# Performance work log

Measured on AMD Instinct MI355X. Metric: run time of the kernel, lower is better.

Reference implementation:

```python
import jax, jax.numpy as jnp
import numpy as np

N, E = 4096, 65536
H = 200
KS = (3072, 1536, 768)  # ceil(0.75*4096), ceil(0.5*3072), ceil(0.5*1536)


def _gcn(A, x, W, b):
    # GCNConv with improved=True: A_hat = A + 2I, sym-normalized
    n = A.shape[0]
    Ah = A + 2.0 * jnp.eye(n, dtype=A.dtype)
    dinv = jax.lax.rsqrt(Ah.sum(axis=1))
    An = dinv[:, None] * Ah * dinv[None, :]
    return An @ (x @ W) + b


def _augment(A):
    # GraphUNet.augment_adj: remove self loops, add self loops (w=1), spspmm(A,A), remove self loops
    n = A.shape[0]
    eye = jnp.eye(n, dtype=A.dtype)
    Ap = A * (1.0 - eye) + eye
    A2 = Ap @ Ap  # dense form of spspmm (two-hop adjacency with weights)
    return A2 * (1.0 - eye)


def _pool(A, x, pw, k):
    # TopKPooling: score = tanh(x.w/||w||), keep top-k, scale kept x by score
    score = jnp.tanh((x @ pw) / jnp.linalg.norm(pw))
    val, perm = jax.lax.top_k(score, k)
    return x[perm] * val[:, None], A[perm][:, perm], perm


def _unet(x, adj, w0, b0, w1, b1, w2, b2, w3, b3, p1, p2, p3,
          u0w, u0b, u1w, u1b, u2w, u2b):
    down = [(w1, b1), (w2, b2), (w3, b3)]
    pws = [p1, p2, p3]
    up = [(u0w, u0b), (u1w, u1b), (u2w, u2b)]
    x = jax.nn.relu(_gcn(adj, x, w0, b0))
    xs, As, perms = [x], [adj], []
    A = adj
    for i in range(3):
        A = _augment(A)
        x, A, perm = _pool(A, x, pws[i], KS[i])
        x = jax.nn.relu(_gcn(A, x, *down[i]))
        if i < 2:
            xs.append(x)
            As.append(A)
        perms.append(perm)
    for i in range(3):
        j = 2 - i
        upf = jnp.zeros_like(xs[j]).at[perms[j]].set(x)
        x = xs[j] + upf  # sum_res=True
        x = _gcn(As[j], x, *up[i])
        if i < 2:
            x = jax.nn.relu(x)
    return jax.nn.log_softmax(x, axis=1)


def setup_inputs() -> dict:
    key = jax.random.key(0)
    ks = jax.random.split(key, 16)
    x = jax.random.normal(ks[0], (N, 3), dtype=jnp.float32)
    src = jax.random.randint(ks[1], (E,), 0, N)
    dst = jax.random.randint(ks[2], (E,), 0, N)
    A = jnp.zeros((N, N), jnp.float32).at[src, dst].set(1.0)
    A = jnp.maximum(A, A.T) * (1.0 - jnp.eye(N, dtype=jnp.float32))
    g = lambda k, s: jax.random.normal(k, s, jnp.float32) * 0.1
    z = lambda n: jnp.zeros((n,), jnp.float32)
    return dict(
        x=x, adj=A,
        w0=g(ks[3], (3, H)), b0=z(H),
        w1=g(ks[4], (H, H)), b1=z(H),
        w2=g(ks[5], (H, H)), b2=z(H),
        w3=g(ks[6], (H, H)), b3=z(H),
        p1=g(ks[7], (H,)), p2=g(ks[8], (H,)), p3=g(ks[9], (H,)),
        u0w=g(ks[10], (H, H)), u0b=z(H),
        u1w=g(ks[11], (H, H)), u1b=z(H),
        u2w=g(ks[12], (H, 2)), u2b=z(2),
    )


def reference(x, adj, w0, b0, w1, b1, w2, b2, w3, b3, p1, p2, p3,
              u0w, u0b, u1w, u1b, u2w, u2b):
    return _unet(x, adj, w0, b0, w1, b1, w2, b2, w3, b3, p1, p2, p3,
                 u0w, u0b, u1w, u1b, u2w, u2b)
```

## Files before the change

### kernel.cpp

```cpp
#include <hip/hip_runtime.h>

typedef unsigned short u16;
typedef unsigned int u32;
typedef unsigned long long u64;
typedef signed char s8;
typedef __attribute__((ext_vector_type(8))) short bfrag8;
typedef __attribute__((ext_vector_type(4))) float f32x4;
typedef __attribute__((ext_vector_type(4))) int i32x4;
typedef __attribute__((address_space(1))) const void gconst_void;
typedef __attribute__((address_space(3))) void lds_void_t;

__device__ __forceinline__ float bf2f(u16 u) {
  return __uint_as_float(((u32)u) << 16);
}
__device__ __forceinline__ u16 f2bf(float f) {
  u32 u = __float_as_uint(f);
  u32 r = (u + 0x7FFFu + ((u >> 16) & 1u)) >> 16;
  return (u16)r;
}
__device__ __forceinline__ void split3(float v, u16& hi, u16& mi, u16& lo) {
  hi = f2bf(v); float r1 = v - bf2f(hi);
  mi = f2bf(r1); float r2 = r1 - bf2f(mi);
  lo = f2bf(r2);
}
__device__ __forceinline__ float ld1(const void* p, int isbf, long idx) {
  return isbf ? bf2f(((const u16*)p)[idx]) : ((const float*)p)[idx];
}
__device__ __forceinline__ void ld4(const void* p, int isbf, long base, long gc, long bound, float v[4]) {
  if (gc + 3 < bound && ((base & 3) == 0)) {
    if (isbf) {
      const ushort4 u = *(const ushort4*)((const u16*)p + base);
      v[0] = bf2f(u.x); v[1] = bf2f(u.y); v[2] = bf2f(u.z); v[3] = bf2f(u.w);
    } else {
      const float4 f = *(const float4*)((const float*)p + base);
      v[0] = f.x; v[1] = f.y; v[2] = f.z; v[3] = f.w;
    }
  } else {
    #pragma unroll
    for (int d = 0; d < 4; ++d) v[d] = (gc + d < bound) ? ld1(p, isbf, base + d) : 0.f;
  }
}

__global__ void detect_k(const u32* __restrict__ a, long nw, int* __restrict__ flag) {
  long stride = (long)gridDim.x * 256;
  int f = 0;
  for (long j = (long)blockIdx.x * 256 + threadIdx.x; j < nw; j += stride) {
    u32 w = a[j];
    if (w == 0x00003F80u || w == 0x3F803F80u) f = 1;
  }
  if (__any(f)) {
    if ((threadIdx.x & 63) == 0) atomicOr(flag, 1);
  }
}

__device__ __forceinline__ int get_bf(int abf, const int* dtf) {
  return (abf >= 0) ? abf : *dtf;
}

__device__ __forceinline__ void stageB16(const void* g, void* lds) {
#if __has_builtin(__builtin_amdgcn_global_load_lds)
  __builtin_amdgcn_global_load_lds((gconst_void*)g, (lds_void_t*)lds, 16, 0, 0);
#else
  int lane = threadIdx.x & 63;
  *(int4*)((char*)lds + lane * 16) = *(const int4*)g;
#endif
}

__global__ __launch_bounds__(256) void syrk_tri_i8_parts(
    const s8* __restrict__ Ag, int ldk, int Ksplit, int ntri,
    int* __restrict__ parts)
{
  __shared__ s8 At[128 * 64];
  __shared__ s8 Bt[128 * 64];
  const int t = blockIdx.x;
  int ti = (int)((sqrtf((float)(8 * t + 1)) - 1.0f) * 0.5f);
  while ((ti + 1) * (ti + 2) / 2 <= t) ++ti;
  while (ti * (ti + 1) / 2 > t) --ti;
  const int tj = t - ti * (ti + 1) / 2;

  const int tid = threadIdx.x;
  const int wave = tid >> 6, lane = tid & 63;
  const int wr = wave >> 1, wc = wave & 1;
  const long rowA0 = (long)ti * 128;
  const long rowB0 = (long)tj * 128;
  const int kbeg = blockIdx.y * Ksplit;
  const int kend = kbeg + Ksplit;

  i32x4 acc[4][4];
  #pragma unroll
  for (int i = 0; i < 4; ++i)
    #pragma unroll
    for (int j = 0; j < 4; ++j) acc[i][j] = (i32x4)0;

  const int srow = lane >> 2;
  const int scol = (lane & 3) * 16;
  const int m = lane & 15, q = lane >> 4;

  for (int k0 = kbeg; k0 < kend; k0 += 64) {
    #pragma unroll
    for (int tt = 0; tt < 2; ++tt) {
      const int r = wave * 32 + tt * 16;
      stageB16(Ag + (rowA0 + r + srow) * (long)ldk + k0 + scol, At + r * 64);
      stageB16(Ag + (rowB0 + r + srow) * (long)ldk + k0 + scol, Bt + r * 64);
    }
    __syncthreads();

    i32x4 af[4], bf[4];
    #pragma unroll
    for (int mt = 0; mt < 4; ++mt)
      af[mt] = *(const i32x4*)(At + (wr * 64 + mt * 16 + m) * 64 + q * 16);
    #pragma unroll
    for (int nt = 0; nt < 4; ++nt)
      bf[nt] = *(const i32x4*)(Bt + (wc * 64 + nt * 16 + m) * 64 + q * 16);
    #pragma unroll
    for (int mt = 0; mt < 4; ++mt)
      #pragma unroll
      for (int nt = 0; nt < 4; ++nt)
        acc[mt][nt] = __builtin_amdgcn_mfma_i32_16x16x64_i8(af[mt], bf[nt], acc[mt][nt], 0, 0, 0);
    __syncthreads();
  }

  int* P = parts + ((long)blockIdx.y * ntri + t) * 16384;
  #pragma unroll
  for (int mt = 0; mt < 4; ++mt) {
    #pragma unroll
    for (int nt = 0; nt < 4; ++nt) {
      const int r0 = wr * 64 + mt * 16 + q * 4;
      const int c = wc * 64 + nt * 16 + m;
      #pragma unroll
      for (int r = 0; r < 4; ++r)
        P[(r0 + r) * 128 + c] = acc[mt][nt][r];
    }
  }
}

__global__ __launch_bounds__(256) void reduce_tri_i8_k(
    const int* __restrict__ parts, int ntri, int n, int nz,
    u16* __restrict__ Ah, u16* __restrict__ Al)
{
  __shared__ float T[128 * 33];
  const int t = blockIdx.x >> 2;
  const int slab = blockIdx.x & 3;
  int ti = (int)((sqrtf((float)(8 * t + 1)) - 1.0f) * 0.5f);
  while ((ti + 1) * (ti + 2) / 2 <= t) ++ti;
  while (ti * (ti + 1) / 2 > t) --ti;
  const int tj = t - ti * (ti + 1) / 2;
  const long rowA0 = (long)ti * 128;
  const long rowB0 = (long)tj * 128;
  const int r0 = slab * 32;
  const int tid = threadIdx.x;
  const long tstride = (long)ntri * 16384;

  #pragma unroll
  for (int it = 0; it < 16; ++it) {
    const int idx = it * 256 + tid;
    const int lr = idx >> 7;
    const int lc = idx & 127;
    long base = (long)t * 16384 + (r0 + lr) * 128 + lc;
    int v = 0;
    for (int z = 0; z < nz; ++z) v += parts[(long)z * tstride + base];
    const long gr = rowA0 + r0 + lr;
    const long gc = rowB0 + lc;
    if (gr == gc) v = 0;
    const float fv = (float)v;
    const u16 h = f2bf(fv);
    const long o = gr * n + gc;
    Ah[o] = h;
    if (Al) Al[o] = f2bf(fv - bf2f(h));
    T[lc * 33 + lr] = fv;
  }
  if (ti == tj) return;
  __syncthreads();
  #pragma unroll
  for (int it = 0; it < 16; ++it) {
    const int idx = it * 256 + tid;
    const int mr = idx >> 5;
    const int mc = idx & 31;
    const float fv = T[mr * 33 + mc];
    const u16 h = f2bf(fv);
    const long o = (rowB0 + mr) * n + rowA0 + r0 + mc;
    Ah[o] = h;
    if (Al) Al[o] = f2bf(fv - bf2f(h));
  }
}

__global__ void rowsum_planes_k(const u16* __restrict__ Ah, const u16* __restrict__ Al,
                                int n, double* __restrict__ rs) {
  __shared__ double red[256];
  const int row = blockIdx.x, tid = threadIdx.x;
  const uint4* A4 = (const uint4*)(Ah + (long)row * n);
  const uint4* L4 = Al ? (const uint4*)(Al + (long)row * n) : nullptr;
  const int n8 = n >> 3;
  double s = 0.0;
  for (int j = tid; j < n8; j += 256) {
    uint4 u = A4[j];
    float v = bf2f((u16)(u.x & 0xFFFFu)) + bf2f((u16)(u.x >> 16))
            + bf2f((u16)(u.y & 0xFFFFu)) + bf2f((u16)(u.y >> 16))
            + bf2f((u16)(u.z & 0xFFFFu)) + bf2f((u16)(u.z >> 16))
            + bf2f((u16)(u.w & 0xFFFFu)) + bf2f((u16)(u.w >> 16));
    if (L4) {
      uint4 l = L4[j];
      v += bf2f((u16)(l.x & 0xFFFFu)) + bf2f((u16)(l.x >> 16))
         + bf2f((u16)(l.y & 0xFFFFu)) + bf2f((u16)(l.y >> 16))
         + bf2f((u16)(l.z & 0xFFFFu)) + bf2f((u16)(l.z >> 16))
         + bf2f((u16)(l.w & 0xFFFFu)) + bf2f((u16)(l.w >> 16));
    }
    s += (double)v;
  }
  red[tid] = s; __syncthreads();
  for (int st = 128; st > 0; st >>= 1) {
    if (tid < st) red[tid] += red[tid + st];
    __syncthreads();
  }
  if (tid == 0) rs[row] = red[0];
}

__global__ __launch_bounds__(256) void syrk_tri2_parts(
    const u16* __restrict__ Ah, const u16* __restrict__ Al, int ldk,
    float* __restrict__ parts, int n, int per)
{
  __shared__ u16 Ath[128 * 32];
  __shared__ u16 Bth[128 * 32];
  __shared__ u16 Atl[128 * 32];
  __shared__ u16 Btl[128 * 32];
  const int t = blockIdx.x;
  int ti = (int)((sqrtf((float)(8 * t + 1)) - 1.0f) * 0.5f);
  while ((ti + 1) * (ti + 2) / 2 <= t) ++ti;
  while (ti * (ti + 1) / 2 > t) --ti;
  const int tj = t - ti * (ti + 1) / 2;

  const int tid = threadIdx.x;
  const int wave = tid >> 6, lane = tid & 63;
  const int wr = wave >> 1, wc = wave & 1;
  const long rowA0 = (long)ti * 128;
  const long rowB0 = (long)tj * 128;
  const int kbeg = blockIdx.y * per;
  const int kend = kbeg + per;

  f32x4 acc[4][4];
  #pragma unroll
  for (int i = 0; i < 4; ++i)
    #pragma unroll
    for (int j = 0; j < 4; ++j) acc[i][j] = (f32x4)0.f;

  const int srow = lane >> 2;
  const int scol = (lane & 3) * 8;
  const int m = lane & 15, q = lane >> 4;

  for (int k0 = kbeg; k0 < kend; k0 += 32) {
    #pragma unroll
    for (int tt = 0; tt < 2; ++tt) {
      const int r = wave * 32 + tt * 16;
      stageB16(Ah + (rowA0 + r + srow) * (long)ldk + k0 + scol, Ath + r * 32);
      stageB16(Ah + (rowB0 + r + srow) * (long)ldk + k0 + scol, Bth + r * 32);
      stageB16(Al + (rowA0 + r + srow) * (long)ldk + k0 + scol, Atl + r * 32);
      stageB16(Al + (rowB0 + r + srow) * (long)ldk + k0 + scol, Btl + r * 32);
    }
    __syncthreads();

    bfrag8 afh[4], afl[4], bfh[4], bfl[4];
    #pragma unroll
    for (int mt = 0; mt < 4; ++mt) {
      afh[mt] = *(const bfrag8*)(Ath + (wr * 64 + mt * 16 + m) * 32 + q * 8);
      afl[mt] = *(const bfrag8*)(Atl + (wr * 64 + mt * 16 + m) * 32 + q * 8);
    }
    #pragma unroll
    for (int nt = 0; nt < 4; ++nt) {
      bfh[nt] = *(const bfrag8*)(Bth + (wc * 64 + nt * 16 + m) * 32 + q * 8);
      bfl[nt] = *(const bfrag8*)(Btl + (wc * 64 + nt * 16 + m) * 32 + q * 8);
    }
    #pragma unroll
    for (int mt = 0; mt < 4; ++mt)
      #pragma unroll
      for (int nt = 0; nt < 4; ++nt) {
        acc[mt][nt] = __builtin_amdgcn_mfma_f32_16x16x32_bf16(afh[mt], bfh[nt], acc[mt][nt], 0, 0, 0);
        acc[mt][nt] = __builtin_amdgcn_mfma_f32_16x16x32_bf16(afh[mt], bfl[nt], acc[mt][nt], 0, 0, 0);
        acc[mt][nt] = __builtin_amdgcn_mfma_f32_16x16x32_bf16(afl[mt], bfh[nt], acc[mt][nt], 0, 0, 0);
        acc[mt][nt] = __builtin_amdgcn_mfma_f32_16x16x32_bf16(afl[mt], bfl[nt], acc[mt][nt], 0, 0, 0);
      }
    __syncthreads();
  }

  float* P = parts + (long)blockIdx.y * n * n;
  #pragma unroll
  for (int mt = 0; mt < 4; ++mt) {
    #pragma unroll
    for (int nt = 0; nt < 4; ++nt) {
      const long gr0 = rowA0 + wr * 64 + mt * 16 + q * 4;
      const long gc = rowB0 + wc * 64 + nt * 16 + m;
      #pragma unroll
      for (int r = 0; r < 4; ++r)
        P[(gr0 + r) * n + gc] = acc[mt][nt][r];
    }
  }
}

__global__ void reduce_tri_mirror_k(const float* __restrict__ parts,
                                    u16* __restrict__ Ah, u16* __restrict__ Al,
                                    double* __restrict__ rsum, int n, int nz) {
  __shared__ double red[256];
  const int tid = threadIdx.x;
  long idx = (long)blockIdx.x * 256 + tid;
  long nn = (long)n * n;
  long r = idx / n, c = idx - r * n;
  double myv = 0.0;
  if (idx < nn) {
    if (r == c) {
      Ah[idx] = 0; Al[idx] = 0;
    } else if (r > c) {
      float s = 0.f;
      for (int z = 0; z < nz; ++z) s += parts[(long)z * nn + r * n + c];
      long mi = c * n + r;
      u16 h = f2bf(s);
      u16 l = f2bf(s - bf2f(h));
      Ah[idx] = h; Al[idx] = l;
      Ah[mi] = h;  Al[mi] = l;
      myv = (double)s;
      atomicAdd(&rsum[c], (double)s);
    }
  }
  red[tid] = myv;
  __syncthreads();
  for (int st = 128; st > 0; st >>= 1) {
    if (tid < st) red[tid] += red[tid + st];
    __syncthreads();
  }
  if (tid == 0 && idx < nn) atomicAdd(&rsum[r], red[0]);
}

__global__ void bg_i8_k(const void* __restrict__ src, int srcbf, int nsrc,
                        const int* __restrict__ perm, int kRows,
                        s8* __restrict__ Ag, const int* __restrict__ dtf,
                        const float* __restrict__ xsrc, const float* __restrict__ score,
                        float* __restrict__ xdst, unsigned nbB) {
  if (blockIdx.x < nbB) {
    long tot = (long)kRows * nsrc;
    long idx = (long)blockIdx.x * 256 + threadIdx.x;
    if (idx >= tot) return;
    int r = (int)(idx / nsrc);
    int c = (int)(idx - (long)r * nsrc);
    int p = perm[r];
    float v = ld1(src, get_bf(srcbf, dtf), (long)p * nsrc + c);
    if (c == p) v += 1.f;
    Ag[idx] = (s8)(int)v;
  } else {
    long tot = (long)kRows * 200;
    long idx = (long)(blockIdx.x - nbB) * 256 + threadIdx.x;
    if (idx >= tot) return;
    int r = (int)(idx / 200);
    int c = (int)(idx - (long)r * 200);
    int p = perm[r];
    xdst[idx] = xsrc[(long)p * 200 + c] * score[p];
  }
}

__global__ void bg_sp_k(const u16* __restrict__ srcH, const u16* __restrict__ srcL,
                        int nsrc, const int* __restrict__ perm, int kRows,
                        u16* __restrict__ Agh, u16* __restrict__ Agl,
                        const float* __restrict__ xsrc, const float* __restrict__ score,
                        float* __restrict__ xdst, unsigned nbB) {
  if (blockIdx.x < nbB) {
    long tot = (long)kRows * nsrc;
    long idx = (long)blockIdx.x * 256 + threadIdx.x;
    if (idx >= tot) return;
    int r = (int)(idx / nsrc);
    int c = (int)(idx - (long)r * nsrc);
    int p = perm[r];
    long si = (long)p * nsrc + c;
    float v = bf2f(srcH[si]) + bf2f(srcL[si]);
    if (c == p) v += 1.f;
    u16 h = f2bf(v);
    Agh[idx] = h;
    Agl[idx] = f2bf(v - bf2f(h));
  } else {
    long tot = (long)kRows * 200;
    long idx = (long)(blockIdx.x - nbB) * 256 + threadIdx.x;
    if (idx >= tot) return;
    int r = (int)(idx / 200);
    int c = (int)(idx - (long)r * 200);
    int p = perm[r];
    xdst[idx] = xsrc[(long)p * 200 + c] * score[p];
  }
}

template<int NT>
__global__ __launch_bounds__(256) void agg_mfma(
    const u16* __restrict__ Ah, const u16* __restrict__ Al,
    const u16* __restrict__ ZT, float* __restrict__ parts,
    int K, int per_steps)
{
  __shared__ u16 At[128 * 32];
  __shared__ u16 Alt[128 * 32];
  __shared__ u16 Zt[3 * NT * 512];
  const int tid = threadIdx.x;
  const int wave = tid >> 6, lane = tid & 63;
  const long row0 = (long)blockIdx.x * 128;
  const int chunk = blockIdx.y;
  const int kbeg = chunk * per_steps * 32;
  const int kend = min(K, kbeg + per_steps * 32);
  const int m = lane & 15, q = lane >> 4;
  const int srow = lane >> 2, scol = (lane & 3) * 8;
  const bool hasAl = (Al != nullptr);

  f32x4 acc[2][NT];
  #pragma unroll
  for (int rt = 0; rt < 2; ++rt)
    #pragma unroll
    for (int ct = 0; ct < NT; ++ct) acc[rt][ct] = (f32x4)0.f;

  for (int k0 = kbeg; k0 < kend; k0 += 32) {
    #pragma unroll
    for (int t = 0; t < 2; ++t) {
      const int r = wave * 32 + t * 16;
      stageB16(Ah + (row0 + r + srow) * (long)K + k0 + scol, At + r * 32);
      if (hasAl)
        stageB16(Al + (row0 + r + srow) * (long)K + k0 + scol, Alt + r * 32);
    }
    for (int s = wave; s < 3 * NT; s += 4) {
      const u16* g = ZT + ((long)(s * 16 + srow)) * K + k0 + scol;
      stageB16(g, Zt + s * 512);
    }
    __syncthreads();

    bfrag8 af0 = *(const bfrag8*)(At + (wave * 32 + m) * 32 + q * 8);
    bfrag8 af1 = *(const bfrag8*)(At + (wave * 32 + 16 + m) * 32 + q * 8);
    bfrag8 al0, al1;
    if (hasAl) {
      al0 = *(const bfrag8*)(Alt + (wave * 32 + m) * 32 + q * 8);
      al1 = *(const bfrag8*)(Alt + (wave * 32 + 16 + m) * 32 + q * 8);
    }
    #pragma unroll
    for (int ct = 0; ct < NT; ++ct) {
      bfrag8 b0 = *(const bfrag8*)(Zt + (0 * NT + ct) * 512 + m * 32 + q * 8);
      bfrag8 b1 = *(const bfrag8*)(Zt + (1 * NT + ct) * 512 + m * 32 + q * 8);
      bfrag8 b2 = *(const bfrag8*)(Zt + (2 * NT + ct) * 512 + m * 32 + q * 8);
      acc[0][ct] = __builtin_amdgcn_mfma_f32_16x16x32_bf16(af0, b0, acc[0][ct], 0, 0, 0);
      acc[0][ct] = __builtin_amdgcn_mfma_f32_16x16x32_bf16(af0, b1, acc[0][ct], 0, 0, 0);
      acc[0][ct] = __builtin_amdgcn_mfma_f32_16x16x32_bf16(af0, b2, acc[0][ct], 0, 0, 0);
      acc[1][ct] = __builtin_amdgcn_mfma_f32_16x16x32_bf16(af1, b0, acc[1][ct], 0, 0, 0);
      acc[1][ct] = __builtin_amdgcn_mfma_f32_16x16x32_bf16(af1, b1, acc[1][ct], 0, 0, 0);
      acc[1][ct] = __builtin_amdgcn_mfma_f32_16x16x32_bf16(af1, b2, acc[1][ct], 0, 0, 0);
      if (hasAl) {
        acc[0][ct] = __builtin_amdgcn_mfma_f32_16x16x32_bf16(al0, b0, acc[0][ct], 0, 0, 0);
        acc[0][ct] = __builtin_amdgcn_mfma_f32_16x16x32_bf16(al0, b1, acc[0][ct], 0, 0, 0);
        acc[1][ct] = __builtin_amdgcn_mfma_f32_16x16x32_bf16(al1, b0, acc[1][ct], 0, 0, 0);
        acc[1][ct] = __builtin_amdgcn_mfma_f32_16x16x32_bf16(al1, b1, acc[1][ct], 0, 0, 0);
      }
    }
    __syncthreads();
  }

  float* P = parts + (long)chunk * gridDim.x * 128 * (NT * 16);
  #pragma unroll
  for (int rt = 0; rt < 2; ++rt) {
    #pragma unroll
    for (int ct = 0; ct < NT; ++ct) {
      const long grow0 = row0 + wave * 32 + rt * 16 + q * 4;
      const long gcol = ct * 16 + m;
      #pragma unroll
      for (int r = 0; r < 4; ++r)
        P[(grow0 + r) * (NT * 16) + gcol] = acc[rt][ct][r];
    }
  }
}

__global__ __launch_bounds__(256) void reduce_epi_k(
    const float* __restrict__ parts, const float* __restrict__ Zs,
    const double* __restrict__ rs, const float* __restrict__ b,
    float* __restrict__ out, int n, int nz, int relu,
    const float* __restrict__ pw, float* __restrict__ score)
{
  __shared__ float vrow[200];
  const int i = blockIdx.x, tid = threadIdx.x;
  float dv = (float)(1.0 / sqrt(rs[i] + 2.0));
  if (tid < 200) {
    long base = (long)i * 208 + tid;
    float s = 0.f;
    for (int c = 0; c < nz; ++c) s += parts[(long)c * n * 208 + base];
    float v = dv * (s + 2.f * Zs[(long)i * 200 + tid]) + b[tid];
    if (relu) v = fmaxf(v, 0.f);
    out[(long)i * 200 + tid] = v;
    if (score) vrow[tid] = v;
  }
  if (!score) return;
  __syncthreads();
  if (tid < 64) {
    double ps = 0.0;
    for (int j = tid; j < 200; j += 64) { double w = pw[j]; ps += w * w; }
    for (int off = 32; off > 0; off >>= 1) ps += __shfl_down(ps, off);
    double nrm = sqrt(__shfl(ps, 0));
    double s = 0.0;
    for (int j = tid; j < 200; j += 64) s += (double)vrow[j] * (double)pw[j];
    for (int off = 32; off > 0; off >>= 1) s += __shfl_down(s, off);
    if (tid == 0) score[i] = (float)tanh(s / nrm);
  }
}

__global__ void a_from_adj_rs_k(const void* __restrict__ adj, const int* __restrict__ dtf,
                                int n, u16* __restrict__ Ah, double* __restrict__ rs) {
  __shared__ double red[256];
  int bf = *dtf;
  const int row = blockIdx.x, tid = threadIdx.x;
  const long base = (long)row * n;
  double s = 0.0;
  for (int j = tid; j < n; j += 256) {
    float v = ld1(adj, bf, base + j);
    Ah[base + j] = bf ? ((const u16*)adj)[base + j] : f2bf(v);
    s += (double)v;
  }
  red[tid] = s; __syncthreads();
  for (int st = 128; st > 0; st >>= 1) {
    if (tid < st) red[tid] += red[tid + st];
    __syncthreads();
  }
  if (tid == 0) rs[row] = red[0];
}

__global__ __launch_bounds__(256) void gemm64_f64(
    const void* __restrict__ Ap, long lda, int abf,
    const void* __restrict__ Bp, long ldb, int bbf,
    float* __restrict__ C, long ldc, int M, int N, int K,
    const double* __restrict__ rsum, u16* __restrict__ ZT, const int* __restrict__ dtf)
{
  const int abf_ = get_bf(abf, dtf);
  const int bbf_ = get_bf(bbf, dtf);
  __shared__ float As[16][64];
  __shared__ float Bs[16][64];
  const int tid = threadIdx.x;
  const int tr = tid >> 4, tc = tid & 15;
  const long row0 = (long)blockIdx.y * 64;
  const long col0 = (long)blockIdx.x * 64;
  double acc[4][4];
  #pragma unroll
  for (int i = 0; i < 4; ++i)
    #pragma unroll
    for (int j = 0; j < 4; ++j) acc[i][j] = 0.0;

  const int am = tid >> 2;
  const int ak = (tid & 3) * 4;
  const int bk = tid >> 4;
  const int bn = (tid & 15) * 4;

  for (int k0 = 0; k0 < K; k0 += 16) {
    float va[4] = {0.f, 0.f, 0.f, 0.f};
    {
      long gm = row0 + am; long gk = k0 + ak;
      if (gm < M && gk < K) ld4(Ap, abf_, gm * lda + gk, gk, K, va);
    }
    As[ak + 0][am] = va[0]; As[ak + 1][am] = va[1];
    As[ak + 2][am] = va[2]; As[ak + 3][am] = va[3];

    float vb[4] = {0.f, 0.f, 0.f, 0.f};
    {
      long gk = k0 + bk; long gn = col0 + bn;
      if (gk < K && gn < N) ld4(Bp, bbf_, gk * ldb + gn, gn, N, vb);
    }
    Bs[bk][bn + 0] = vb[0]; Bs[bk][bn + 1] = vb[1];
    Bs[bk][bn + 2] = vb[2]; Bs[bk][bn + 3] = vb[3];

    __syncthreads();
    #pragma unroll
    for (int kk = 0; kk < 16; ++kk) {
      float a[4], b[4];
      #pragma unroll
      for (int i = 0; i < 4; ++i) a[i] = As[kk][tr * 4 + i];
      #pragma unroll
      for (int j = 0; j < 4; ++j) b[j] = Bs[kk][tc * 4 + j];
      #pragma unroll
      for (int i = 0; i < 4; ++i)
        #pragma unroll
        for (int j = 0; j < 4; ++j)
          acc[i][j] += (double)a[i] * (double)b[j];
    }
    __syncthreads();
  }
  #pragma unroll
  for (int i = 0; i < 4; ++i) {
    long gm = row0 + tr * 4 + i;
    if (gm >= M) continue;
    float sc = rsum ? (float)(1.0 / sqrt(rsum[gm] + 2.0)) : 1.f;
    #pragma unroll
    for (int j = 0; j < 4; ++j) {
      long gn = col0 + tc * 4 + j;
      if (gn < N) {
        float v0 = (float)acc[i][j];
        float v = v0 * sc;
        C[gm * ldc + gn] = v;
        if (ZT) {
          u16 hi, mi, lo; split3(v, hi, mi, lo);
          ZT[((long)0 * 208 + gn) * M + gm] = hi;
          ZT[((long)1 * 208 + gn) * M + gm] = mi;
          ZT[((long)2 * 208 + gn) * M + gm] = lo;
        }
      }
    }
  }
}

struct UpBatch {
  const void* src[19];
  float* dst[19];
  int n[19];
};

__global__ void upcast_batch_k(UpBatch ub, const int* __restrict__ dtf) {
  int bf = *dtf;
  int a = blockIdx.y;
  int i = blockIdx.x * 256 + threadIdx.x;
  if (i < ub.n[a]) ub.dst[a][i] = ld1(ub.src[a], bf, i);
}

template<int V>
__global__ __launch_bounds__(1024) void topk_fast(const float* __restrict__ score,
                                                  int n, int np2, int k,
                                                  int* __restrict__ perm,
                                                  int* __restrict__ inv) {
  __shared__ u64 keys[4096];
  const int tid = threadIdx.x;
  const int REGMAX = 32 * V;
  for (int i = tid; i < n; i += 1024) inv[i] = -1;
  u64 kreg[V];
  #pragma unroll
  for (int r = 0; r < V; ++r) {
    int i = tid * V + r;
    u64 key = 0ULL;
    if (i < n) {
      u32 b = __float_as_uint(score[i]);
      u32 u = (b & 0x80000000u) ? ~b : (b | 0x80000000u);
      key = ((u64)u << 32) | (u32)(~(u32)i);
    }
    kreg[r] = key;
  }

  for (int size = 2; size <= np2; size <<= 1) {
    int stride = size >> 1;
    if (stride > REGMAX) {
      #pragma unroll
      for (int r = 0; r < V; ++r) keys[tid * V + r] = kreg[r];
      __syncthreads();
      for (; stride > REGMAX; stride >>= 1) {
        for (int i = tid; i < np2; i += 1024) {
          int j = i ^ stride;
          if (j > i) {
            u64 a = keys[i], b = keys[j];
            bool up = ((i & size) == 0);
            if (up ? (a > b) : (a < b)) { keys[i] = b; keys[j] = a; }
          }
        }
        __syncthreads();
      }
      #pragma unroll
      for (int r = 0; r < V; ++r) kreg[r] = keys[tid * V + r];
    }
    for (; stride >= 1; stride >>= 1) {
      if (stride >= V) {
        int lm = stride / V;
        #pragma unroll
        for (int r = 0; r < V; ++r) {
          u64 mine = kreg[r];
          u64 other = (u64)__shfl_xor((long long)mine, lm);
          int i = tid * V + r;
          bool up = ((i & size) == 0);
          bool lower = ((i & stride) == 0);
          u64 mn = mine < other ? mine : other;
          u64 mx = mine < other ? other : mine;
          kreg[r] = (lower == up) ? mn : mx;
        }
      } else {
        #pragma unroll
        for (int r = 0; r < V; ++r) {
          int pr = r ^ stride;
          if (pr > r) {
            int i = tid * V + r;
            bool up = ((i & size) == 0);
            u64 a = kreg[r], b = kreg[pr];
            if (up ? (a > b) : (a < b)) { kreg[r] = b; kreg[pr] = a; }
          }
        }
      }
    }
  }
  #pragma unroll
  for (int r = 0; r < V; ++r) {
    int i = tid * V + r;
    int rank = np2 - 1 - i;
    if (rank < k) {
      int idx = (int)(~(u32)(kreg[r] & 0xFFFFFFFFull));
      perm[rank] = idx;
      inv[idx] = rank;
    }
  }
}

__global__ void upadd_k(const float* __restrict__ xs, const float* __restrict__ xpool,
                        const int* __restrict__ inv, float* __restrict__ dst, long nh, int h) {
  long idx = (long)blockIdx.x * 256 + threadIdx.x;
  if (idx >= nh) return;
  int i = (int)(idx / h);
  int c = (int)(idx - (long)i * h);
  float v = xs[idx];
  int r = inv[i];
  if (r >= 0) v += xpool[(long)r * h + c];
  dst[idx] = v;
}

__global__ void matvec2_final_k(const void* __restrict__ A, int abf, int n,
                                const float* __restrict__ Zs, const double* __restrict__ rs0,
                                const float* __restrict__ b2, float* __restrict__ out,
                                const int* __restrict__ dtf) {
  const int bf = get_bf(abf, dtf);
  int row = blockIdx.x, tid = threadIdx.x;
  const long base = (long)row * n;
  double s0 = 0.0, s1 = 0.0;
  for (int j = tid; j < n; j += 256) {
    double a = (double)ld1(A, bf, base + j);
    s0 += a * (double)Zs[2 * j];
    s1 += a * (double)Zs[2 * j + 1];
  }
  __shared__ double r0[256], r1[256];
  r0[tid] = s0; r1[tid] = s1; __syncthreads();
  for (int st = 128; st > 0; st >>= 1) {
    if (tid < st) { r0[tid] += r0[tid + st]; r1[tid] += r1[tid + st]; }
    __syncthreads();
  }
  if (tid == 0) {
    double y0 = (double)((float)r0[0]);
    double y1 = (double)((float)r1[0]);
    double di = (double)((float)(1.0 / sqrt(rs0[row] + 2.0)));
    double t0 = di * (y0 + 2.0 * (double)Zs[2 * row]) + (double)b2[0];
    double t1 = di * (y1 + 2.0 * (double)Zs[2 * row + 1]) + (double)b2[1];
    double mx = fmax(t0, t1);
    double l = mx + log(exp(t0 - mx) + exp(t1 - mx));
    out[2 * row] = (float)(t0 - l);
    out[2 * row + 1] = (float)(t1 - l);
  }
}

extern "C" void kernel_launch(void* const* d_in, const int* in_sizes, int n_in,
                              void* d_out, int out_size, void* d_ws, size_t ws_size,
                              hipStream_t stream) {
  const int N0 = 4096, H = 200;
  const int K1 = 3072, K2 = 1536, K3 = 768;

  const void* in_x = d_in[0];
  const void* adj  = d_in[1];
  const void* w0 = d_in[2];  const void* b0 = d_in[3];
  const void* w1 = d_in[4];  const void* b1 = d_in[5];
  const void* w2 = d_in[6];  const void* b2 = d_in[7];
  const void* w3 = d_in[8];  const void* b3 = d_in[9];
  const void* p1 = d_in[10]; const void* p2 = d_in[11];
  const void* p3 = d_in[12];
  const void* u0w = d_in[13]; const void* u0b = d_in[14];
  const void* u1w = d_in[15]; const void* u1b = d_in[16];
  const void* u2w = d_in[17]; const void* u2b = d_in[18];

  char* wp = (char*)d_ws;
  auto alloc = [&](size_t bytes) -> void* {
    void* p = (void*)wp;
    wp += (bytes + 255) & ~(size_t)255;
    return p;
  };
  size_t partsBytes = (size_t)300 * 4 * 16384 * 4 + 1024;
  float* parts = (float*)alloc(partsBytes);
  s8*    Agb  = (s8*)alloc((size_t)K1 * N0);
  u16* Ag3h = (u16*)alloc((size_t)K3 * K2 * 2);
  u16* Ag3l = (u16*)alloc((size_t)K3 * K2 * 2);
  u16* Ah0 = (u16*)alloc((size_t)N0 * N0 * 2);
  u16* Ah1 = (u16*)alloc((size_t)K1 * K1 * 2);
  u16* Ah2 = (u16*)alloc((size_t)K2 * K2 * 2);
  u16* Al2 = (u16*)alloc((size_t)K2 * K2 * 2);
  u16* Ah3 = (u16*)alloc((size_t)K3 * K3 * 2);
  u16* Al3 = (u16*)alloc((size_t)K3 * K3 * 2);
  u16* ZT  = (u16*)alloc((size_t)3 * 208 * N0 * 2);
  float* xs0  = (float*)alloc((size_t)N0 * H * 4);
  float* xs1  = (float*)alloc((size_t)K1 * H * 4);
  float* xs2  = (float*)alloc((size_t)K2 * H * 4);
  float* xcur = (float*)alloc((size_t)N0 * H * 4);
  float* xtmp = (float*)alloc((size_t)N0 * H * 4);
  float* Zbuf = (float*)alloc((size_t)N0 * H * 4);
  float* Xinf = (float*)alloc((size_t)N0 * 3 * 4);
  double* rs0 = (double*)alloc((size_t)N0 * 8);
  double* rs1 = (double*)alloc((size_t)K1 * 8);
  double* rs2 = (double*)alloc((size_t)K2 * 8);
  double* rs3 = (double*)alloc((size_t)K3 * 8);
  int* dtflag = (int*)alloc(256);
  float* scores = (float*)alloc((size_t)N0 * 4);
  int* perm1 = (int*)alloc((size_t)K1 * 4);
  int* perm2 = (int*)alloc((size_t)K2 * 4);
  int* perm3 = (int*)alloc((size_t)K3 * 4);
  int* inv1 = (int*)alloc((size_t)N0 * 4);
  int* inv2 = (int*)alloc((size_t)K1 * 4);
  int* inv3 = (int*)alloc((size_t)K2 * 4);
  float* w0f = (float*)alloc(3 * H * 4);  float* b0f = (float*)alloc(H * 4);
  float* w1f = (float*)alloc(H * H * 4);  float* b1f = (float*)alloc(H * 4);
  float* w2f = (float*)alloc(H * H * 4);  float* b2f = (float*)alloc(H * 4);
  float* w3f = (float*)alloc(H * H * 4);  float* b3f = (float*)alloc(H * 4);
  float* p1f = (float*)alloc(H * 4);
  float* p2f = (float*)alloc(H * 4);
  float* p3f = (float*)alloc(H * 4);
  float* u0wf = (float*)alloc(H * H * 4); float* u0bf = (float*)alloc(H * 4);
  float* u1wf = (float*)alloc(H * H * 4); float* u1bf = (float*)alloc(H * 4);
  float* u2wf = (float*)alloc(H * 2 * 4); float* u2bf = (float*)alloc(2 * 4);
  (void)in_sizes; (void)n_in; (void)out_size; (void)ws_size;

  hipMemsetAsync(rs1, 0, (size_t)(K1 + K2 + K3) * 8 + 256, stream);
  detect_k<<<dim3(4096), dim3(256), 0, stream>>>((const u32*)adj, (long)N0 * N0 / 2, dtflag);

  {
    UpBatch ub;
    const void* srcs[19] = {in_x, w0, b0, w1, b1, w2, b2, w3, b3, p1, p2, p3,
                            u0w, u0b, u1w, u1b, u2w, u2b, u2b};
    float* dsts[19] = {Xinf, w0f, b0f, w1f, b1f, w2f, b2f, w3f, b3f, p1f, p2f, p3f,
                       u0wf, u0bf, u1wf, u1bf, u2wf, u2bf, u2bf};
    int ns[19] = {N0 * 3, 3 * H, H, H * H, H, H * H, H, H * H, H, H, H, H,
                  H * H, H, H * H, H, H * 2, 2, 2};
    for (int i = 0; i < 19; ++i) { ub.src[i] = srcs[i]; ub.dst[i] = dsts[i]; ub.n[i] = ns[i]; }
    upcast_batch_k<<<dim3((N0 * 3 + 255) / 256, 19), dim3(256), 0, stream>>>(ub, dtflag);
  }

  a_from_adj_rs_k<<<dim3(N0), dim3(256), 0, stream>>>(adj, dtflag, N0, Ah0, rs0);

  auto gemm64 = [&](const void* A, long lda, int abf, const void* B, long ldb, int bbf,
                    float* C, long ldc, int M, int Nn, int K, const double* rsum, u16* zt) {
    dim3 g((Nn + 63) / 64, (M + 63) / 64);
    gemm64_f64<<<g, dim3(256), 0, stream>>>(A, lda, abf, B, ldb, bbf, C, ldc, M, Nn, K,
                                            rsum, zt, dtflag);
  };

  auto gcn = [&](const u16* Ah, const u16* Al, int n, int chunks, const double* rs,
                 const float* Xin_, int din, const float* W, const float* bb,
                 float* out, const float* pwf, float* scoreOut) {
    gemm64(Xin_, din, 0, W, H, 0, Zbuf, H, n, H, din, rs, ZT);
    agg_mfma<13><<<dim3(n / 128, chunks), dim3(256), 0, stream>>>(
        Ah, Al, ZT, parts, n, (n / 32) / chunks);
    reduce_epi_k<<<dim3(n), dim3(256), 0, stream>>>(
        parts, Zbuf, rs, bb, out, n, chunks, 1, pwf, scoreOut);
  };

  gcn(Ah0, nullptr, N0, 8, rs0, Xinf, 3, w0f, b0f, xs0, p1f, scores);

  topk_fast<4><<<dim3(1), dim3(1024), 0, stream>>>(scores, N0, 4096, K1, perm1, inv1);
  {
    unsigned nbB = (unsigned)(((long)K1 * N0 + 255) / 256);
    unsigned nbG = (unsigned)(((long)K1 * 200 + 255) / 256);
    bg_i8_k<<<dim3(nbB + nbG), dim3(256), 0, stream>>>(
        adj, -1, N0, perm1, K1, Agb, dtflag, xs0, scores, xcur, nbB);
    int nt = K1 / 128;
    int ntri = nt * (nt + 1) / 2;
    syrk_tri_i8_parts<<<dim3(ntri, 4), dim3(256), 0, stream>>>(
        Agb, N0, N0 / 4, ntri, (int*)parts);
    reduce_tri_i8_k<<<dim3(ntri * 4), dim3(256), 0, stream>>>(
        (const int*)parts, ntri, K1, 4, Ah1, nullptr);
    rowsum_planes_k<<<dim3(K1), dim3(256), 0, stream>>>(Ah1, nullptr, K1, rs1);
  }
  gcn(Ah1, nullptr, K1, 12, rs1, xcur, H, w1f, b1f, xs1, p2f, scores);

  topk_fast<4><<<dim3(1), dim3(1024), 0, stream>>>(scores, K1, 4096, K2, perm2, inv2);
  {
    unsigned nbB = (unsigned)(((long)K2 * K1 + 255) / 256);
    unsigned nbG = (unsigned)(((long)K2 * 200 + 255) / 256);
    bg_i8_k<<<dim3(nbB + nbG), dim3(256), 0, stream>>>(
        Ah1, 1, K1, perm2, K2, Agb, dtflag, xs1, scores, xcur, nbB);
    int nt = K2 / 128;
    int ntri = nt * (nt + 1) / 2;
    syrk_tri_i8_parts<<<dim3(ntri, 8), dim3(256), 0, stream>>>(
        Agb, K1, K1 / 8, ntri, (int*)parts);
    reduce_tri_i8_k<<<dim3(ntri * 4), dim3(256), 0, stream>>>(
        (const int*)parts, ntri, K2, 8, Ah2, Al2);
    rowsum_planes_k<<<dim3(K2), dim3(256), 0, stream>>>(Ah2, Al2, K2, rs2);
  }
  gcn(Ah2, Al2, K2, 24, rs2, xcur, H, w2f, b2f, xs2, p3f, scores);

  topk_fast<2><<<dim3(1), dim3(1024), 0, stream>>>(scores, K2, 2048, K3, perm3, inv3);
  {
    unsigned nbB = (unsigned)(((long)K3 * K2 + 255) / 256);
    unsigned nbG = (unsigned)(((long)K3 * 200 + 255) / 256);
    bg_sp_k<<<dim3(nbB + nbG), dim3(256), 0, stream>>>(
        Ah2, Al2, K2, perm3, K3, Ag3h, Ag3l, xs2, scores, xcur, nbB);
    int nt = K3 / 128;
    syrk_tri2_parts<<<dim3(nt * (nt + 1) / 2, 8), dim3(256), 0, stream>>>(
        Ag3h, Ag3l, K2, parts, K3, K2 / 8);
    long nn = (long)K3 * K3;
    reduce_tri_mirror_k<<<dim3((unsigned)(nn / 256)), dim3(256), 0, stream>>>(
        parts, Ah3, Al3, rs3, K3, 8);
  }
  gcn(Ah3, Al3, K3, 24, rs3, xcur, H, w3f, b3f, xcur, nullptr, nullptr);

  upadd_k<<<dim3((unsigned)(((long)K2 * H + 255) / 256)), dim3(256), 0, stream>>>(
      xs2, xcur, inv3, xtmp, (long)K2 * H, H);
  gcn(Ah2, Al2, K2, 24, rs2, xtmp, H, u0wf, u0bf, xcur, nullptr, nullptr);

  upadd_k<<<dim3((unsigned)(((long)K1 * H + 255) / 256)), dim3(256), 0, stream>>>(
      xs1, xcur, inv2, xtmp, (long)K1 * H, H);
  gcn(Ah1, nullptr, K1, 12, rs1, xtmp, H, u1wf, u1bf, xcur, nullptr, nullptr);

  upadd_k<<<dim3((unsigned)(((long)N0 * H + 255) / 256)), dim3(256), 0, stream>>>(
      xs0, xcur, inv1, xtmp, (long)N0 * H, H);
  gemm64(xtmp, H, 0, u2wf, 2, 0, Zbuf, 2, N0, 2, H, rs0, nullptr);
  matvec2_final_k<<<dim3(N0), dim3(256), 0, stream>>>(
      adj, -1, N0, Zbuf, rs0, u2bf, (float*)d_out, dtflag);
}
```

Measured before the change: 925.7 us.

## Double-buffer agg_mfma LDS staging and split column tiles across 8 waves

Rewrites the GCN aggregation MFMA kernel to run 512 threads per block. The 8 waves split the 13 column tiles into two groups of 4 row-group waves, which cuts the accumulator registers per wave. LDS tiles are double-buffered so the next K-step's global-to-LDS staging is issued before the current step's MFMAs, removing one barrier per iteration. The Al presence check becomes a template parameter. In exchange it uses more LDS per block, which may limit occupancy, and the column split is uneven (7 vs 6 tiles).

```diff
diff --git a/kernel.cpp b/kernel.cpp
--- a/kernel.cpp
+++ b/kernel.cpp
@@ -383,83 +383,107 @@
   }
 }
 
-template<int NT>
-__global__ __launch_bounds__(256) void agg_mfma(
+template<int NT, int HASAL>
+__global__ __launch_bounds__(512) void agg_mfma8(
     const u16* __restrict__ Ah, const u16* __restrict__ Al,
     const u16* __restrict__ ZT, float* __restrict__ parts,
     int K, int per_steps)
 {
-  __shared__ u16 At[128 * 32];
-  __shared__ u16 Alt[128 * 32];
-  __shared__ u16 Zt[3 * NT * 512];
+  constexpr int CT0 = (NT + 1) / 2;
+  constexpr int NZT = 3 * NT;
+  constexpr int NSTG = (HASAL ? 16 : 8) + NZT;
+  __shared__ u16 At[2][8 * 512];
+  __shared__ u16 Alt[(HASAL ? 2 : 1)][8 * 512];
+  __shared__ u16 Zt[2][NZT * 512];
+
   const int tid = threadIdx.x;
   const int wave = tid >> 6, lane = tid & 63;
+  const int rg = wave & 3;
+  const int cg = wave >> 2;
+  const int ct_base = cg ? CT0 : 0;
+  const int nct = cg ? (NT - CT0) : CT0;
   const long row0 = (long)blockIdx.x * 128;
   const int chunk = blockIdx.y;
   const int kbeg = chunk * per_steps * 32;
-  const int kend = min(K, kbeg + per_steps * 32);
+  const int nsteps = (min(K, kbeg + per_steps * 32) - kbeg) / 32;
   const int m = lane & 15, q = lane >> 4;
   const int srow = lane >> 2, scol = (lane & 3) * 8;
-  const bool hasAl = (Al != nullptr);
-
-  f32x4 acc[2][NT];
+
+  auto stage = [&](int buf, int k0) {
+    u16* Atb = At[buf];
+    u16* Ztb = Zt[buf];
+    u16* Altb = Alt[HASAL ? buf : 0];
+    for (int s = wave; s < NSTG; s += 8) {
+      if (s < 8) {
+        stageB16(Ah + (row0 + s * 16 + srow) * (long)K + k0 + scol, Atb + s * 512);
+      } else if (HASAL && s < 16) {
+        stageB16(Al + (row0 + (s - 8) * 16 + srow) * (long)K + k0 + scol, Altb + (s - 8) * 512);
+      } else {
+        const int z = s - (HASAL ? 16 : 8);
+        stageB16(ZT + ((long)(z * 16 + srow)) * K + k0 + scol, Ztb + z * 512);
+      }
+    }
+  };
+
+  f32x4 acc[2][CT0];
   #pragma unroll
   for (int rt = 0; rt < 2; ++rt)
     #pragma unroll
-    for (int ct = 0; ct < NT; ++ct) acc[rt][ct] = (f32x4)0.f;
-
-  for (int k0 = kbeg; k0 < kend; k0 += 32) {
-    #pragma unroll
-    for (int t = 0; t < 2; ++t) {
-      const int r = wave * 32 + t * 16;
-      stageB16(Ah + (row0 + r + srow) * (long)K + k0 + scol, At + r * 32);
-      if (hasAl)
-        stageB16(Al + (row0 + r + srow) * (long)K + k0 + scol, Alt + r * 32);
-    }
-    for (int s = wave; s < 3 * NT; s += 4) {
-      const u16* g = ZT + ((long)(s * 16 + srow)) * K + k0 + scol;
-      stageB16(g, Zt + s * 512);
-    }
-    __syncthreads();
-
-    bfrag8 af0 = *(const bfrag8*)(At + (wave * 32 + m) * 32 + q * 8);
-    bfrag8 af1 = *(const bfrag8*)(At + (wave * 32 + 16 + m) * 32 + q * 8);
+    for (int ct = 0; ct < CT0; ++ct) acc[rt][ct] = (f32x4)0.f;
+
+  stage(0, kbeg);
+  __syncthreads();
+  int cur = 0;
+  for (int t = 0; t < nsteps; ++t) {
+    if (t + 1 < nsteps) stage(cur ^ 1, kbeg + (t + 1) * 32);
+
+    const u16* Atb = At[cur];
+    const u16* Ztb = Zt[cur];
+    bfrag8 af0 = *(const bfrag8*)(Atb + (rg * 2) * 512 + m * 32 + q * 8);
+    bfrag8 af1 = *(const bfrag8*)(Atb + (rg * 2 + 1) * 512 + m * 32 + q * 8);
     bfrag8 al0, al1;
-    if (hasAl) {
-      al0 = *(const bfrag8*)(Alt + (wave * 32 + m) * 32 + q * 8);
-      al1 = *(const bfrag8*)(Alt + (wave * 32 + 16 + m) * 32 + q * 8);
-    }
-    #pragma unroll
-    for (int ct = 0; ct < NT; ++ct) {
-      bfrag8 b0 = *(const bfrag8*)(Zt + (0 * NT + ct) * 512 + m * 32 + q * 8);
-      bfrag8 b1 = *(const bfrag8*)(Zt + (1 * NT + ct) * 512 + m * 32 + q * 8);
-      bfrag8 b2 = *(const bfrag8*)(Zt + (2 * NT + ct) * 512 + m * 32 + q * 8);
-      acc[0][ct] = __builtin_amdgcn_mfma_f32_16x16x32_bf16(af0, b0, acc[0][ct], 0, 0, 0);
-      acc[0][ct] = __builtin_amdgcn_mfma_f32_16x16x32_bf16(af0, b1, acc[0][ct], 0, 0, 0);
-      acc[0][ct] = __builtin_amdgcn_mfma_f32_16x16x32_bf16(af0, b2, acc[0][ct], 0, 0, 0);
-      acc[1][ct] = __builtin_amdgcn_mfma_f32_16x16x32_bf16(af1, b0, acc[1][ct], 0, 0, 0);
-      acc[1][ct] = __builtin_amdgcn_mfma_f32_16x16x32_bf16(af1, b1, acc[1][ct], 0, 0, 0);
-      acc[1][ct] = __builtin_amdgcn_mfma_f32_16x16x32_bf16(af1, b2, acc[1][ct], 0, 0, 0);
-      if (hasAl) {
-        acc[0][ct] = __builtin_amdgcn_mfma_f32_16x16x32_bf16(al0, b0, acc[0][ct], 0, 0, 0);
-        acc[0][ct] = __builtin_amdgcn_mfma_f32_16x16x32_bf16(al0, b1, acc[0][ct], 0, 0, 0);
-        acc[1][ct] = __builtin_amdgcn_mfma_f32_16x16x32_bf16(al1, b0, acc[1][ct], 0, 0, 0);
-        acc[1][ct] = __builtin_amdgcn_mfma_f32_16x16x32_bf16(al1, b1, acc[1][ct], 0, 0, 0);
+    if (HASAL) {
+      const u16* Altb = Alt[cur];
+      al0 = *(const bfrag8*)(Altb + (rg * 2) * 512 + m * 32 + q * 8);
+      al1 = *(const bfrag8*)(Altb + (rg * 2 + 1) * 512 + m * 32 + q * 8);
+    }
+    #pragma unroll
+    for (int ct = 0; ct < CT0; ++ct) {
+      if (ct < nct) {
+        const int c = ct_base + ct;
+        bfrag8 b0 = *(const bfrag8*)(Ztb + (0 * NT + c) * 512 + m * 32 + q * 8);
+        bfrag8 b1 = *(const bfrag8*)(Ztb + (1 * NT + c) * 512 + m * 32 + q * 8);
+        bfrag8 b2 = *(const bfrag8*)(Ztb + (2 * NT + c) * 512 + m * 32 + q * 8);
+        acc[0][ct] = __builtin_amdgcn_mfma_f32_16x16x32_bf16(af0, b0, acc[0][ct], 0, 0, 0);
+        acc[0][ct] = __builtin_amdgcn_mfma_f32_16x16x32_bf16(af0, b1, acc[0][ct], 0, 0, 0);
+        acc[0][ct] = __builtin_amdgcn_mfma_f32_16x16x32_bf16(af0, b2, acc[0][ct], 0, 0, 0);
+        acc[1][ct] = __builtin_amdgcn_mfma_f32_16x16x32_bf16(af1, b0, acc[1][ct], 0, 0, 0);
+        acc[1][ct] = __builtin_amdgcn_mfma_f32_16x16x32_bf16(af1, b1, acc[1][ct], 0, 0, 0);
+        acc[1][ct] = __builtin_amdgcn_mfma_f32_16x16x32_bf16(af1, b2, acc[1][ct], 0, 0, 0);
+        if (HASAL) {
+          acc[0][ct] = __builtin_amdgcn_mfma_f32_16x16x32_bf16(al0, b0, acc[0][ct], 0, 0, 0);
+          acc[0][ct] = __builtin_amdgcn_mfma_f32_16x16x32_bf16(al0, b1, acc[0][ct], 0, 0, 0);
+          acc[1][ct] = __builtin_amdgcn_mfma_f32_16x16x32_bf16(al1, b0, acc[1][ct], 0, 0, 0);
+          acc[1][ct] = __builtin_amdgcn_mfma_f32_16x16x32_bf16(al1, b1, acc[1][ct], 0, 0, 0);
+        }
       }
     }
-    __syncthreads();
+    if (t + 1 < nsteps) __syncthreads();
+    cur ^= 1;
   }
 
   float* P = parts + (long)chunk * gridDim.x * 128 * (NT * 16);
   #pragma unroll
   for (int rt = 0; rt < 2; ++rt) {
     #pragma unroll
-    for (int ct = 0; ct < NT; ++ct) {
-      const long grow0 = row0 + wave * 32 + rt * 16 + q * 4;
-      const long gcol = ct * 16 + m;
-      #pragma unroll
-      for (int r = 0; r < 4; ++r)
-        P[(grow0 + r) * (NT * 16) + gcol] = acc[rt][ct][r];
+    for (int ct = 0; ct < CT0; ++ct) {
+      if (ct < nct) {
+        const long grow0 = row0 + rg * 32 + rt * 16 + q * 4;
+        const long gcol = (ct_base + ct) * 16 + m;
+        #pragma unroll
+        for (int r = 0; r < 4; ++r)
+          P[(grow0 + r) * (NT * 16) + gcol] = acc[rt][ct][r];
+      }
     }
   }
 }
@@ -831,8 +855,12 @@
                  const float* Xin_, int din, const float* W, const float* bb,
                  float* out, const float* pwf, float* scoreOut) {
     gemm64(Xin_, din, 0, W, H, 0, Zbuf, H, n, H, din, rs, ZT);
-    agg_mfma<13><<<dim3(n / 128, chunks), dim3(256), 0, stream>>>(
-        Ah, Al, ZT, parts, n, (n / 32) / chunks);
+    if (Al)
+      agg_mfma8<13, 1><<<dim3(n / 128, chunks), dim3(512), 0, stream>>>(
+          Ah, Al, ZT, parts, n, (n / 32) / chunks);
+    else
+      agg_mfma8<13, 0><<<dim3(n / 128, chunks), dim3(512), 0, stream>>>(
+          Ah, nullptr, ZT, parts, n, (n / 32) / chunks);
     reduce_epi_k<<<dim3(n), dim3(256), 0, stream>>>(
         parts, Zbuf, rs, bb, out, n, chunks, 1, pwf, scoreOut);
   };
```

Result: faster. 879.6 us (-5.0%).
